# Optimization experiments

Measured on AMD Instinct MI355X. Metric: run time of the kernel, lower is better.

Reference implementation:

```python
import jax, jax.numpy as jnp
import numpy as np

T, N, E = 12, 10000, 320000
IN_DIM, HID_DIM, EMB_DIM = 64, 128, 64


def setup_inputs() -> dict:
    key = jax.random.key(0)
    ks = jax.random.split(key, 12)
    s1 = 1.0 / np.sqrt(IN_DIM)
    s2 = 1.0 / np.sqrt(HID_DIM)
    sg = 1.0 / np.sqrt(EMB_DIM)
    return {
        "x_seq": jax.random.normal(ks[0], (T, N, IN_DIM), dtype=jnp.float32),
        "edge_index": jax.random.randint(ks[1], (2, E), 0, N, dtype=jnp.int64),
        "edge_weight": jax.random.uniform(ks[2], (E,), dtype=jnp.float32),
        # GCNConv layer 1 (weight stored as [in, out])
        "W1": jax.random.uniform(ks[3], (IN_DIM, HID_DIM), minval=-s1, maxval=s1, dtype=jnp.float32),
        "b1": jnp.zeros((HID_DIM,), dtype=jnp.float32),
        # GCNConv layer 2
        "W2": jax.random.uniform(ks[4], (HID_DIM, EMB_DIM), minval=-s2, maxval=s2, dtype=jnp.float32),
        "b2": jnp.zeros((EMB_DIM,), dtype=jnp.float32),
        # GRU params (torch layout: [3H, in] with gate order r, z, n)
        "W_ih": jax.random.uniform(ks[5], (3 * EMB_DIM, EMB_DIM), minval=-sg, maxval=sg, dtype=jnp.float32),
        "W_hh": jax.random.uniform(ks[6], (3 * EMB_DIM, EMB_DIM), minval=-sg, maxval=sg, dtype=jnp.float32),
        "b_ih": jax.random.uniform(ks[7], (3 * EMB_DIM,), minval=-sg, maxval=sg, dtype=jnp.float32),
        "b_hh": jax.random.uniform(ks[8], (3 * EMB_DIM,), minval=-sg, maxval=sg, dtype=jnp.float32),
        "dec_bias": jnp.zeros((1,), dtype=jnp.float32),
    }


def _gcn_conv(x, W, b, row, col, ew, n):
    # PyG GCNConv with self-loops already appended to (row, col, ew).
    deg = jax.ops.segment_sum(ew, col, num_segments=n)  # [N]
    dinv = jnp.where(deg > 0, jax.lax.rsqrt(jnp.where(deg > 0, deg, 1.0)), 0.0)
    norm = dinv[row] * ew * dinv[col]                   # [E+N]
    h = x @ W                                           # [N, out]
    agg = jax.ops.segment_sum(h[row] * norm[:, None], col, num_segments=n)
    return agg + b


def reference(x_seq, edge_index, edge_weight, W1, b1, W2, b2, W_ih, W_hh, b_ih, b_hh, dec_bias):
    n = x_seq.shape[1]
    loop = jnp.arange(n, dtype=edge_index.dtype)
    row = jnp.concatenate([edge_index[0], loop])
    col = jnp.concatenate([edge_index[1], loop])
    ew = jnp.concatenate([edge_weight, jnp.ones((n,), dtype=edge_weight.dtype)])

    def encode(x):  # x: [N, in_dim]
        h = jax.nn.relu(_gcn_conv(x, W1, b1, row, col, ew, n))
        # dropout p=0.3 only active in training; eval -> identity
        return _gcn_conv(h, W2, b2, row, col, ew, n)  # [N, emb]

    z_seq = jax.vmap(encode)(x_seq)  # [T, N, emb]

    emb = z_seq.shape[-1]

    def gru_step(h, xt):
        gi = xt @ W_ih.T + b_ih      # [N, 3H]
        gh = h @ W_hh.T + b_hh       # [N, 3H]
        i_r, i_z, i_n = jnp.split(gi, 3, axis=-1)
        h_r, h_z, h_n = jnp.split(gh, 3, axis=-1)
        r = jax.nn.sigmoid(i_r + h_r)
        zg = jax.nn.sigmoid(i_z + h_z)
        ng = jnp.tanh(i_n + r * h_n)
        h_new = (1.0 - zg) * ng + zg * h
        return h_new, None

    h0 = jnp.zeros((n, emb), dtype=x_seq.dtype)
    z, _ = jax.lax.scan(gru_step, h0, z_seq)  # out[-1] == final hidden state

    od_pred = jax.nn.softplus(z @ z.T + dec_bias)  # [N, N]
    return od_pred, z
```

## Files before the change

### kernel.cpp

```cpp
#include <hip/hip_runtime.h>
#include <cstdint>
#include <cstddef>

#define T_STEPS 12
#define NNODES  10000
#define NEDGES  320000
#define IN_DIM  64
#define HID     128
#define EMB     64
#define G3      192
#define NPAD    10112

typedef __attribute__((ext_vector_type(8))) short short8;
typedef __attribute__((ext_vector_type(4))) float f32x4;

__global__ void k_setup(float* __restrict__ deg, int* __restrict__ cnt) {
    int i = blockIdx.x * 256 + threadIdx.x;
    if (i < NNODES) { deg[i] = 1.0f; cnt[i] = 1; }
}

__global__ void k_edge(const int* __restrict__ eidx, const float* __restrict__ ew,
                       float* __restrict__ deg, int* __restrict__ cnt) {
    int e = blockIdx.x * 256 + threadIdx.x;
    if (e >= NEDGES) return;
    int c = eidx[NEDGES + e];
    atomicAdd(&deg[c], ew[e]);
    atomicAdd(&cnt[c], 1);
}

__global__ void k_dinv(const float* __restrict__ deg, float* __restrict__ dinv) {
    int i = blockIdx.x * 256 + threadIdx.x;
    if (i >= NNODES) return;
    float d = deg[i];
    dinv[i] = (d > 0.0f) ? rsqrtf(d) : 0.0f;
}

__global__ __launch_bounds__(1024) void k_scan(const int* __restrict__ cnt,
                                               int* __restrict__ offs, int* __restrict__ cursor) {
    __shared__ int sh[1024];
    int t = threadIdx.x;
    int loc[10];
    int run = 0;
#pragma unroll
    for (int i = 0; i < 10; ++i) {
        int idx = t * 10 + i;
        int v = (idx < NNODES) ? cnt[idx] : 0;
        loc[i] = run;
        run += v;
    }
    sh[t] = run;
    __syncthreads();
    for (int off = 1; off < 1024; off <<= 1) {
        int v = 0;
        if (t >= off) v = sh[t - off];
        __syncthreads();
        if (t >= off) sh[t] += v;
        __syncthreads();
    }
    int base = (t > 0) ? sh[t - 1] : 0;
#pragma unroll
    for (int i = 0; i < 10; ++i) {
        int idx = t * 10 + i;
        if (idx < NNODES) {
            int e = base + loc[i];
            offs[idx] = e;
            cursor[idx] = e;
        }
    }
    if (t == 1023) offs[NNODES] = sh[1023];
}

__global__ void k_scatter(const int* __restrict__ eidx, const float* __restrict__ ew,
                          const float* __restrict__ dinv, int* __restrict__ cursor,
                          int* __restrict__ srcb, float* __restrict__ wnb) {
    int e = blockIdx.x * 256 + threadIdx.x;
    if (e < NEDGES) {
        int r = eidx[e];
        int c = eidx[NEDGES + e];
        float w = dinv[r] * ew[e] * dinv[c];
        int p = atomicAdd(&cursor[c], 1);
        srcb[p] = r; wnb[p] = w;
    } else if (e < NEDGES + NNODES) {
        int i = e - NEDGES;
        float di = dinv[i];
        int p = atomicAdd(&cursor[i], 1);
        srcb[p] = i; wnb[p] = di * di;
    }
}

template <int K, int NO, int GR, int RPT, bool BT, bool BIAS, bool PERM>
__global__ __launch_bounds__(NO* GR) void k_mm(const float* __restrict__ A,
                                               const float* __restrict__ B,
                                               const float* __restrict__ bias,
                                               float* __restrict__ C, int M) {
    constexpr int NOP = NO + 1;
    __shared__ float Bs[K * NOP];
    const int tid = threadIdx.x;
    constexpr int NTHR = NO * GR;
    for (int i = tid; i < K * NO; i += NTHR) {
        if (BT) { int k = i / NO, c = i - k * NO; Bs[k * NOP + c] = B[i]; }
        else    { int c = i / K,  k = i - c * K;  Bs[k * NOP + c] = B[i]; }
    }
    __syncthreads();
    const int c  = tid % NO;
    const int rg = tid / NO;
    const float bv = BIAS ? bias[c] : 0.0f;
    for (int r0 = (blockIdx.x * GR + rg) * RPT; r0 < M; r0 += gridDim.x * GR * RPT) {
        int r0u = __builtin_amdgcn_readfirstlane(r0);
        float acc[RPT];
#pragma unroll
        for (int i = 0; i < RPT; ++i) acc[i] = bv;
        const float4* A4 = (const float4*)A + (size_t)r0u * (K / 4);
        for (int k0 = 0; k0 < K; k0 += 4) {
            float a[RPT][4];
#pragma unroll
            for (int i = 0; i < RPT; ++i) {
                float4 v = A4[i * (K / 4) + (k0 >> 2)];
                a[i][0] = v.x; a[i][1] = v.y; a[i][2] = v.z; a[i][3] = v.w;
            }
#pragma unroll
            for (int j = 0; j < 4; ++j) {
                float b = Bs[(k0 + j) * NOP + c];
#pragma unroll
                for (int i = 0; i < RPT; ++i) acc[i] = fmaf(a[i][j], b, acc[i]);
            }
        }
#pragma unroll
        for (int i = 0; i < RPT; ++i) {
            int rr = r0 + i;
            size_t orow = PERM ? ((size_t)(rr % NNODES) * T_STEPS + rr / NNODES) : (size_t)rr;
            C[orow * NO + c] = acc[i];
        }
    }
}

template <int F, bool RELU>
__global__ __launch_bounds__(256) void k_agg(const float* __restrict__ H,
                                             const int* __restrict__ srcb,
                                             const float* __restrict__ wnb,
                                             const int* __restrict__ offs,
                                             const float* __restrict__ bias,
                                             float* __restrict__ out) {
    int node = (blockIdx.x * 256 + threadIdx.x) >> 6;
    node = __builtin_amdgcn_readfirstlane(node);
    if (node >= NNODES) return;
    int lane = threadIdx.x & 63;
    int beg = offs[node], end = offs[node + 1];
    if (F == 128) {
        const float2* H2 = (const float2*)H;
        float2 bv = ((const float2*)bias)[lane];
        float2 acc[T_STEPS];
#pragma unroll
        for (int t = 0; t < T_STEPS; ++t) acc[t] = bv;
        for (int e0 = beg; e0 < end; e0 += 64) {
            int idx = e0 + lane;
            int sv = (idx < end) ? srcb[idx] : 0;
            float wv = (idx < end) ? wnb[idx] : 0.0f;
            int m = min(64, end - e0);
            for (int j = 0; j < m; ++j) {
                int sj = __shfl(sv, j);
                float wj = __shfl(wv, j);
                size_t base = (size_t)sj * (T_STEPS * 64);
#pragma unroll
                for (int t = 0; t < T_STEPS; ++t) {
                    float2 hv = H2[base + t * 64 + lane];
                    acc[t].x = fmaf(wj, hv.x, acc[t].x);
                    acc[t].y = fmaf(wj, hv.y, acc[t].y);
                }
            }
        }
        float2* O2 = (float2*)out;
#pragma unroll
        for (int t = 0; t < T_STEPS; ++t) {
            float2 a = acc[t];
            if (RELU) { a.x = fmaxf(a.x, 0.0f); a.y = fmaxf(a.y, 0.0f); }
            O2[((size_t)node * T_STEPS + t) * 64 + lane] = a;
        }
    } else {
        float bv = bias[lane];
        float acc[T_STEPS];
#pragma unroll
        for (int t = 0; t < T_STEPS; ++t) acc[t] = bv;
        for (int e0 = beg; e0 < end; e0 += 64) {
            int idx = e0 + lane;
            int sv = (idx < end) ? srcb[idx] : 0;
            float wv = (idx < end) ? wnb[idx] : 0.0f;
            int m = min(64, end - e0);
            for (int j = 0; j < m; ++j) {
                int sj = __shfl(sv, j);
                float wj = __shfl(wv, j);
                size_t base = (size_t)sj * (T_STEPS * 64);
#pragma unroll
                for (int t = 0; t < T_STEPS; ++t) {
                    acc[t] = fmaf(wj, H[base + t * 64 + lane], acc[t]);
                }
            }
        }
#pragma unroll
        for (int t = 0; t < T_STEPS; ++t) {
            float a = acc[t];
            if (RELU) a = fmaxf(a, 0.0f);
            out[((size_t)node * T_STEPS + t) * 64 + lane] = a;
        }
    }
}

__global__ __launch_bounds__(192, 3) void k_gru(const float* __restrict__ gi,
                                                const float* __restrict__ W_hh,
                                                const float* __restrict__ b_hh,
                                                float* __restrict__ hout) {
    constexpr int RPB = 6;
    __shared__ float ghs[RPB][G3 + 1];
    __shared__ float hs[RPB][64];
    int tid = threadIdx.x;
    float wv[64];
    const float4* W4 = (const float4*)(W_hh + (size_t)tid * 64);
#pragma unroll
    for (int j = 0; j < 16; ++j) {
        float4 v = W4[j];
        wv[4 * j + 0] = v.x; wv[4 * j + 1] = v.y;
        wv[4 * j + 2] = v.z; wv[4 * j + 3] = v.w;
    }
    for (int i = tid; i < RPB * 64; i += 192) ((float*)hs)[i] = 0.0f;
    __syncthreads();
    int r0 = blockIdx.x * RPB;
    float bh = b_hh[tid];
    for (int t = 0; t < T_STEPS; ++t) {
        float acc[RPB];
#pragma unroll
        for (int i = 0; i < RPB; ++i) acc[i] = bh;
#pragma unroll
        for (int k0 = 0; k0 < 64; k0 += 4) {
#pragma unroll
            for (int i = 0; i < RPB; ++i) {
                float4 h4 = *(const float4*)&hs[i][k0];
                acc[i] = fmaf(h4.x, wv[k0 + 0], acc[i]);
                acc[i] = fmaf(h4.y, wv[k0 + 1], acc[i]);
                acc[i] = fmaf(h4.z, wv[k0 + 2], acc[i]);
                acc[i] = fmaf(h4.w, wv[k0 + 3], acc[i]);
            }
        }
#pragma unroll
        for (int i = 0; i < RPB; ++i) ghs[i][tid] = acc[i];
        __syncthreads();
#pragma unroll
        for (int it = 0; it < 2; ++it) {
            int item = it * 192 + tid;
            int rr = item >> 6, f = item & 63;
            int grow = r0 + rr;
            if (grow < NNODES) {
                const float* gir = gi + ((size_t)grow * T_STEPS + t) * G3;
                float ir = gir[f], iz = gir[64 + f], inn = gir[128 + f];
                float hr = ghs[rr][f], hz = ghs[rr][64 + f], hn = ghs[rr][128 + f];
                float rg = 1.0f / (1.0f + expf(-(ir + hr)));
                float zg = 1.0f / (1.0f + expf(-(iz + hz)));
                float ng = tanhf(fmaf(rg, hn, inn));
                float hp = hs[rr][f];
                hs[rr][f] = fmaf(zg, hp - ng, ng);
            }
        }
        __syncthreads();
    }
#pragma unroll
    for (int it = 0; it < 2; ++it) {
        int item = it * 192 + tid;
        int rr = item >> 6, f = item & 63;
        int grow = r0 + rr;
        if (grow < NNODES) hout[(size_t)grow * 64 + f] = hs[rr][f];
    }
}

__global__ void k_zcopy(const float* __restrict__ h, float* __restrict__ out) {
    int i = blockIdx.x * 256 + threadIdx.x;
    if (i < NNODES * EMB) out[(size_t)NNODES * NNODES + i] = h[i];
}

__global__ void k_zsplit(const float* __restrict__ h,
                         unsigned short* __restrict__ zhi, unsigned short* __restrict__ zlo) {
    int i = blockIdx.x * 256 + threadIdx.x;
    if (i >= NPAD * EMB) return;
    float x = (i < NNODES * EMB) ? h[i] : 0.0f;
    uint32_t b = __float_as_uint(x);
    uint32_t rh = (b + 0x7FFFu + ((b >> 16) & 1u)) & 0xFFFF0000u;
    float fhi = __uint_as_float(rh);
    float lo = x - fhi;
    uint32_t bl = __float_as_uint(lo);
    uint32_t rl = (bl + 0x7FFFu + ((bl >> 16) & 1u)) & 0xFFFF0000u;
    zhi[i] = (unsigned short)(rh >> 16);
    zlo[i] = (unsigned short)(rl >> 16);
}

__device__ __forceinline__ float softplus_fast(float x) {
    float e = __builtin_amdgcn_exp2f(-1.4426950408889634f * fabsf(x));
    float l = 0.6931471805599453f * __builtin_amdgcn_logf(1.0f + e);
    return fmaxf(x, 0.0f) + l;
}

__global__ __launch_bounds__(256) void k_dec(const unsigned short* __restrict__ zhi,
                                             const unsigned short* __restrict__ zlo,
                                             const float* __restrict__ dbias,
                                             float* __restrict__ out) {
    union DecSmem {
        struct { short A[128 * 128]; short B[128 * 128]; } ab;
        float C[128 * 128];
    };
    __shared__ DecSmem sm;
    int tid = threadIdx.x;
    int r0 = blockIdx.y * 128, c0 = blockIdx.x * 128;
    const float4* zh4 = (const float4*)zhi;
    const float4* zl4 = (const float4*)zlo;
#pragma unroll
    for (int p8 = 0; p8 < 8; ++p8) {
        int idx = p8 * 256 + tid;
        int row = idx >> 4, c = idx & 15;
        float4 va = (c < 8) ? zh4[(size_t)(r0 + row) * 8 + c] : zl4[(size_t)(r0 + row) * 8 + (c - 8)];
        float4 vb = (c < 8) ? zh4[(size_t)(c0 + row) * 8 + c] : zl4[(size_t)(c0 + row) * 8 + (c - 8)];
        int pos = c ^ (row & 15);
        *(float4*)&sm.ab.A[row * 128 + pos * 8] = va;
        *(float4*)&sm.ab.B[row * 128 + pos * 8] = vb;
    }
    __syncthreads();
    int lane = tid & 63, w = tid >> 6;
    int r = lane & 15, q = lane >> 4;
    f32x4 acc[2][8];
#pragma unroll
    for (int mt = 0; mt < 2; ++mt)
#pragma unroll
        for (int nt = 0; nt < 8; ++nt) acc[mt][nt] = (f32x4){0.f, 0.f, 0.f, 0.f};
    const int aSel[6] = {0, 4, 0, 4, 8, 12};
    const int bSel[6] = {0, 4, 8, 12, 0, 4};
#pragma unroll
    for (int ks = 0; ks < 6; ++ks) {
        short8 af[2], bf[8];
#pragma unroll
        for (int mt = 0; mt < 2; ++mt) {
            int rowA = w * 32 + mt * 16 + r;
            af[mt] = *(const short8*)&sm.ab.A[rowA * 128 + ((aSel[ks] + q) ^ r) * 8];
        }
#pragma unroll
        for (int nt = 0; nt < 8; ++nt) {
            int rowB = nt * 16 + r;
            bf[nt] = *(const short8*)&sm.ab.B[rowB * 128 + ((bSel[ks] + q) ^ r) * 8];
        }
#pragma unroll
        for (int mt = 0; mt < 2; ++mt)
#pragma unroll
            for (int nt = 0; nt < 8; ++nt)
                acc[mt][nt] = __builtin_amdgcn_mfma_f32_16x16x32_bf16(af[mt], bf[nt], acc[mt][nt], 0, 0, 0);
    }
    float db = dbias[0];
    __syncthreads();
#pragma unroll
    for (int mt = 0; mt < 2; ++mt) {
        int rowb = w * 32 + mt * 16 + q * 4;
#pragma unroll
        for (int nt = 0; nt < 8; ++nt) {
            int col = nt * 16 + r;
#pragma unroll
            for (int reg = 0; reg < 4; ++reg) {
                int row = rowb + reg;
                sm.C[row * 128 + (col ^ ((row & 4) << 2))] = softplus_fast(acc[mt][nt][reg] + db);
            }
        }
    }
    __syncthreads();
    bool full = (r0 + 128 <= NNODES) && (c0 + 128 <= NNODES);
    if (full) {
#pragma unroll
        for (int p = 0; p < 16; ++p) {
            int idx = p * 256 + tid;
            int row = idx >> 5, k = idx & 31;
            float4 v = *(const float4*)&sm.C[row * 128 + ((k * 4) ^ ((row & 4) << 2))];
            *(float4*)&out[(size_t)(r0 + row) * NNODES + c0 + k * 4] = v;
        }
    } else {
        for (int p = 0; p < 16; ++p) {
            int idx = p * 256 + tid;
            int row = idx >> 5, k = idx & 31;
            int gr = r0 + row;
            int gc = c0 + k * 4;
            if (gr >= NNODES || gc >= NNODES) continue;
            float4 v = *(const float4*)&sm.C[row * 128 + ((k * 4) ^ ((row & 4) << 2))];
            if (gc + 4 <= NNODES) {
                *(float4*)&out[(size_t)gr * NNODES + gc] = v;
            } else {
                float vv[4] = {v.x, v.y, v.z, v.w};
                for (int j = 0; j < 4 && gc + j < NNODES; ++j)
                    out[(size_t)gr * NNODES + gc + j] = vv[j];
            }
        }
    }
}

extern "C" void kernel_launch(void* const* d_in, const int* in_sizes, int n_in,
                              void* d_out, int out_size, void* d_ws, size_t ws_size,
                              hipStream_t stream) {
    const float* x_seq = (const float*)d_in[0];
    const int*   eidx  = (const int*)d_in[1];
    const float* ew    = (const float*)d_in[2];
    const float* W1    = (const float*)d_in[3];
    const float* b1    = (const float*)d_in[4];
    const float* W2    = (const float*)d_in[5];
    const float* b2    = (const float*)d_in[6];
    const float* W_ih  = (const float*)d_in[7];
    const float* W_hh  = (const float*)d_in[8];
    const float* b_ih  = (const float*)d_in[9];
    const float* b_hh  = (const float*)d_in[10];
    const float* dbias = (const float*)d_in[11];
    float* out = (float*)d_out;

    char* wsp = (char*)d_ws;
    auto alloc = [&](size_t bytes) {
        char* p = wsp;
        wsp += (bytes + 255) & ~(size_t)255;
        return p;
    };
    float* deg    = (float*)alloc((size_t)NNODES * 4);
    float* dinv   = (float*)alloc((size_t)NNODES * 4);
    int*   cnt    = (int*)alloc((size_t)NNODES * 4);
    int*   offs   = (int*)alloc((size_t)(NNODES + 1) * 4);
    int*   cursor = (int*)alloc((size_t)NNODES * 4);
    int*   srcb   = (int*)alloc((size_t)(NEDGES + NNODES) * 4);
    float* wnb    = (float*)alloc((size_t)(NEDGES + NNODES) * 4);
    float* hst    = (float*)alloc((size_t)NNODES * EMB * 4);
    unsigned short* zhi = (unsigned short*)alloc((size_t)NPAD * EMB * 2);
    unsigned short* zlo = (unsigned short*)alloc((size_t)NPAD * EMB * 2);
    float* Buf1   = (float*)alloc((size_t)T_STEPS * NNODES * G3 * 4);
    float* Buf2   = (float*)alloc((size_t)T_STEPS * NNODES * HID * 4);

    const int M = T_STEPS * NNODES;

    k_setup<<<(NNODES + 255) / 256, 256, 0, stream>>>(deg, cnt);
    k_edge<<<(NEDGES + 255) / 256, 256, 0, stream>>>(eidx, ew, deg, cnt);
    k_dinv<<<(NNODES + 255) / 256, 256, 0, stream>>>(deg, dinv);
    k_scan<<<1, 1024, 0, stream>>>(cnt, offs, cursor);
    k_scatter<<<(NEDGES + NNODES + 255) / 256, 256, 0, stream>>>(eidx, ew, dinv, cursor, srcb, wnb);

    k_mm<64, 128, 2, 8, true, false, true><<<1024, 256, 0, stream>>>(x_seq, W1, nullptr, Buf1, M);
    k_agg<128, true><<<(NNODES * 64 + 255) / 256, 256, 0, stream>>>(Buf1, srcb, wnb, offs, b1, Buf2);
    k_mm<128, 64, 4, 8, true, false, false><<<1024, 256, 0, stream>>>(Buf2, W2, nullptr, Buf1, M);
    k_agg<64, false><<<(NNODES * 64 + 255) / 256, 256, 0, stream>>>(Buf1, srcb, wnb, offs, b2, Buf2);
    k_mm<64, 192, 1, 8, false, true, false><<<1024, 192, 0, stream>>>(Buf2, W_ih, b_ih, Buf1, M);
    k_gru<<<(NNODES + 5) / 6, 192, 0, stream>>>(Buf1, W_hh, b_hh, hst);
    k_zcopy<<<(NNODES * EMB + 255) / 256, 256, 0, stream>>>(hst, out);
    k_zsplit<<<(NPAD * EMB + 255) / 256, 256, 0, stream>>>(hst, zhi, zlo);
    dim3 gdec(NPAD / 128, NPAD / 128);
    k_dec<<<gdec, 256, 0, stream>>>(zhi, zlo, dbias, out);
}
```

Baseline: 1.283 ms.

## Aggregate before first GCN matmul, go time-major, pack edge data

Layer 1 of the GCN is reordered to aggregate the 64-wide input features first and then multiply by W1, using associativity (A·X)·W = A·(X·W). The 128-wide gather is replaced by a 64-wide one, with bias and ReLU fused into the matmul. All buffers switch from node-major with a T-permute to time-major, with a 2D grid of (nodes, timestep) for aggregation. Source index and weight are packed into one int2 per edge so a single load fetches both. Per-timestep aggregation gives up the reuse of each loaded edge across all 12 timesteps and reloads edge data 12 times.

```diff
diff --git a/kernel.cpp b/kernel.cpp
--- a/kernel.cpp
+++ b/kernel.cpp
@@ -72,23 +72,23 @@
 
 __global__ void k_scatter(const int* __restrict__ eidx, const float* __restrict__ ew,
                           const float* __restrict__ dinv, int* __restrict__ cursor,
-                          int* __restrict__ srcb, float* __restrict__ wnb) {
+                          int2* __restrict__ edata) {
     int e = blockIdx.x * 256 + threadIdx.x;
     if (e < NEDGES) {
         int r = eidx[e];
         int c = eidx[NEDGES + e];
         float w = dinv[r] * ew[e] * dinv[c];
         int p = atomicAdd(&cursor[c], 1);
-        srcb[p] = r; wnb[p] = w;
+        edata[p] = make_int2(r, __float_as_int(w));
     } else if (e < NEDGES + NNODES) {
         int i = e - NEDGES;
         float di = dinv[i];
         int p = atomicAdd(&cursor[i], 1);
-        srcb[p] = i; wnb[p] = di * di;
-    }
-}
-
-template <int K, int NO, int GR, int RPT, bool BT, bool BIAS, bool PERM>
+        edata[p] = make_int2(i, __float_as_int(di * di));
+    }
+}
+
+template <int K, int NO, int GR, int RPT, bool BT, bool BIAS, bool RELU>
 __global__ __launch_bounds__(NO* GR) void k_mm(const float* __restrict__ A,
                                                const float* __restrict__ B,
                                                const float* __restrict__ bias,
@@ -127,82 +127,41 @@
         }
 #pragma unroll
         for (int i = 0; i < RPT; ++i) {
-            int rr = r0 + i;
-            size_t orow = PERM ? ((size_t)(rr % NNODES) * T_STEPS + rr / NNODES) : (size_t)rr;
-            C[orow * NO + c] = acc[i];
-        }
-    }
-}
-
-template <int F, bool RELU>
-__global__ __launch_bounds__(256) void k_agg(const float* __restrict__ H,
-                                             const int* __restrict__ srcb,
-                                             const float* __restrict__ wnb,
-                                             const int* __restrict__ offs,
-                                             const float* __restrict__ bias,
-                                             float* __restrict__ out) {
+            float v = acc[i];
+            if (RELU) v = fmaxf(v, 0.0f);
+            C[(size_t)(r0 + i) * NO + c] = v;
+        }
+    }
+}
+
+template <bool BIAS>
+__global__ __launch_bounds__(256) void k_aggt(const float* __restrict__ H,
+                                              const int2* __restrict__ edata,
+                                              const int* __restrict__ offs,
+                                              const float* __restrict__ bias,
+                                              float* __restrict__ out) {
     int node = (blockIdx.x * 256 + threadIdx.x) >> 6;
     node = __builtin_amdgcn_readfirstlane(node);
     if (node >= NNODES) return;
+    int t = blockIdx.y;
     int lane = threadIdx.x & 63;
+    const float* Ht = H + (size_t)t * (NNODES * EMB);
     int beg = offs[node], end = offs[node + 1];
-    if (F == 128) {
-        const float2* H2 = (const float2*)H;
-        float2 bv = ((const float2*)bias)[lane];
-        float2 acc[T_STEPS];
-#pragma unroll
-        for (int t = 0; t < T_STEPS; ++t) acc[t] = bv;
-        for (int e0 = beg; e0 < end; e0 += 64) {
-            int idx = e0 + lane;
-            int sv = (idx < end) ? srcb[idx] : 0;
-            float wv = (idx < end) ? wnb[idx] : 0.0f;
-            int m = min(64, end - e0);
-            for (int j = 0; j < m; ++j) {
-                int sj = __shfl(sv, j);
-                float wj = __shfl(wv, j);
-                size_t base = (size_t)sj * (T_STEPS * 64);
-#pragma unroll
-                for (int t = 0; t < T_STEPS; ++t) {
-                    float2 hv = H2[base + t * 64 + lane];
-                    acc[t].x = fmaf(wj, hv.x, acc[t].x);
-                    acc[t].y = fmaf(wj, hv.y, acc[t].y);
-                }
-            }
-        }
-        float2* O2 = (float2*)out;
-#pragma unroll
-        for (int t = 0; t < T_STEPS; ++t) {
-            float2 a = acc[t];
-            if (RELU) { a.x = fmaxf(a.x, 0.0f); a.y = fmaxf(a.y, 0.0f); }
-            O2[((size_t)node * T_STEPS + t) * 64 + lane] = a;
-        }
-    } else {
-        float bv = bias[lane];
-        float acc[T_STEPS];
-#pragma unroll
-        for (int t = 0; t < T_STEPS; ++t) acc[t] = bv;
-        for (int e0 = beg; e0 < end; e0 += 64) {
-            int idx = e0 + lane;
-            int sv = (idx < end) ? srcb[idx] : 0;
-            float wv = (idx < end) ? wnb[idx] : 0.0f;
-            int m = min(64, end - e0);
-            for (int j = 0; j < m; ++j) {
-                int sj = __shfl(sv, j);
-                float wj = __shfl(wv, j);
-                size_t base = (size_t)sj * (T_STEPS * 64);
-#pragma unroll
-                for (int t = 0; t < T_STEPS; ++t) {
-                    acc[t] = fmaf(wj, H[base + t * 64 + lane], acc[t]);
-                }
-            }
-        }
-#pragma unroll
-        for (int t = 0; t < T_STEPS; ++t) {
-            float a = acc[t];
-            if (RELU) a = fmaxf(a, 0.0f);
-            out[((size_t)node * T_STEPS + t) * 64 + lane] = a;
-        }
-    }
+    float acc = BIAS ? bias[lane] : 0.0f;
+    for (int e0 = beg; e0 < end; e0 += 64) {
+        int idx = e0 + lane;
+        int2 ed = (idx < end) ? edata[idx] : make_int2(0, 0);
+        int sv = ed.x;
+        float wv = __int_as_float(ed.y);
+        int m = min(64, end - e0);
+#pragma unroll 4
+        for (int j = 0; j < m; ++j) {
+            int sj = __shfl(sv, j);
+            float wj = __shfl(wv, j);
+            acc = fmaf(wj, Ht[sj * EMB + lane], acc);
+        }
+    }
+    out[(size_t)t * (NNODES * EMB) + (size_t)node * EMB + lane] = acc;
 }
 
 __global__ __launch_bounds__(192, 3) void k_gru(const float* __restrict__ gi,
@@ -249,7 +208,7 @@
             int rr = item >> 6, f = item & 63;
             int grow = r0 + rr;
             if (grow < NNODES) {
-                const float* gir = gi + ((size_t)grow * T_STEPS + t) * G3;
+                const float* gir = gi + ((size_t)t * NNODES + grow) * G3;
                 float ir = gir[f], iz = gir[64 + f], inn = gir[128 + f];
                 float hr = ghs[rr][f], hz = ghs[rr][64 + f], hn = ghs[rr][128 + f];
                 float rg = 1.0f / (1.0f + expf(-(ir + hr)));
@@ -420,8 +379,7 @@
     int*   cnt    = (int*)alloc((size_t)NNODES * 4);
     int*   offs   = (int*)alloc((size_t)(NNODES + 1) * 4);
     int*   cursor = (int*)alloc((size_t)NNODES * 4);
-    int*   srcb   = (int*)alloc((size_t)(NEDGES + NNODES) * 4);
-    float* wnb    = (float*)alloc((size_t)(NEDGES + NNODES) * 4);
+    int2*  edata  = (int2*)alloc((size_t)(NEDGES + NNODES) * 8);
     float* hst    = (float*)alloc((size_t)NNODES * EMB * 4);
     unsigned short* zhi = (unsigned short*)alloc((size_t)NPAD * EMB * 2);
     unsigned short* zlo = (unsigned short*)alloc((size_t)NPAD * EMB * 2);
@@ -429,19 +387,25 @@
     float* Buf2   = (float*)alloc((size_t)T_STEPS * NNODES * HID * 4);
 
     const int M = T_STEPS * NNODES;
+    float* xa = Buf2;
+    float* g2 = Buf2 + (size_t)T_STEPS * NNODES * EMB;
+    float* z  = Buf2;
+    float* h1 = Buf1;
+    float* gi = Buf1;
 
     k_setup<<<(NNODES + 255) / 256, 256, 0, stream>>>(deg, cnt);
     k_edge<<<(NEDGES + 255) / 256, 256, 0, stream>>>(eidx, ew, deg, cnt);
     k_dinv<<<(NNODES + 255) / 256, 256, 0, stream>>>(deg, dinv);
     k_scan<<<1, 1024, 0, stream>>>(cnt, offs, cursor);
-    k_scatter<<<(NEDGES + NNODES + 255) / 256, 256, 0, stream>>>(eidx, ew, dinv, cursor, srcb, wnb);
-
-    k_mm<64, 128, 2, 8, true, false, true><<<1024, 256, 0, stream>>>(x_seq, W1, nullptr, Buf1, M);
-    k_agg<128, true><<<(NNODES * 64 + 255) / 256, 256, 0, stream>>>(Buf1, srcb, wnb, offs, b1, Buf2);
-    k_mm<128, 64, 4, 8, true, false, false><<<1024, 256, 0, stream>>>(Buf2, W2, nullptr, Buf1, M);
-    k_agg<64, false><<<(NNODES * 64 + 255) / 256, 256, 0, stream>>>(Buf1, srcb, wnb, offs, b2, Buf2);
-    k_mm<64, 192, 1, 8, false, true, false><<<1024, 192, 0, stream>>>(Buf2, W_ih, b_ih, Buf1, M);
-    k_gru<<<(NNODES + 5) / 6, 192, 0, stream>>>(Buf1, W_hh, b_hh, hst);
+    k_scatter<<<(NEDGES + NNODES + 255) / 256, 256, 0, stream>>>(eidx, ew, dinv, cursor, edata);
+
+    dim3 gagg((NNODES * 64 + 255) / 256, T_STEPS);
+    k_aggt<false><<<gagg, 256, 0, stream>>>(x_seq, edata, offs, nullptr, xa);
+    k_mm<64, 128, 2, 8, true, true, true><<<1024, 256, 0, stream>>>(xa, W1, b1, h1, M);
+    k_mm<128, 64, 4, 8, true, false, false><<<1024, 256, 0, stream>>>(h1, W2, nullptr, g2, M);
+    k_aggt<true><<<gagg, 256, 0, stream>>>(g2, edata, offs, b2, z);
+    k_mm<64, 192, 1, 8, false, true, false><<<1024, 192, 0, stream>>>(z, W_ih, b_ih, gi, M);
+    k_gru<<<(NNODES + 5) / 6, 192, 0, stream>>>(gi, W_hh, b_hh, hst);
     k_zcopy<<<(NNODES * EMB + 255) / 256, 256, 0, stream>>>(hst, out);
     k_zsplit<<<(NPAD * EMB + 255) / 256, 256, 0, stream>>>(hst, zhi, zlo);
     dim3 gdec(NPAD / 128, NPAD / 128);
```

Measured after the change: 1.210 ms. -5.7%, faster.
